# Performance work log

Measured on AMD Instinct MI355X. Metric: run time of the kernel, lower is better.

## Reference

```python
import jax, jax.numpy as jnp
import numpy as np

# dims: bs, closeness, nodes, top-k neighbors, model dim, heads, ffn dim
BS, CLOSE, N, K, D, H, FF = 4, 8, 8192, 16, 64, 4, 256
DH = D // H  # per-head dim


def setup_inputs() -> dict:
    key = jax.random.key(0)
    ks = jax.random.split(key, 7)
    w = lambda k, shp: jax.random.normal(k, shp, jnp.float32) * 0.05
    return {
        "x_c": jax.random.normal(ks[0], (BS, CLOSE, 2, N), jnp.float32),
        "W_emb": w(ks[1], (CLOSE, D)),
        "W_qkv": w(ks[2], (3, D, D)),
        "W_o": w(ks[3], (D, D)),
        "W_ff1": w(ks[4], (D, FF)),
        "W_ff2": w(ks[5], (FF, D)),
        "W_out": w(ks[6], (D, CLOSE)),
    }


def _layernorm(x):
    m = jnp.mean(x, -1, keepdims=True)
    v = jnp.var(x, -1, keepdims=True)
    return (x - m) * jax.lax.rsqrt(v + 1e-5)


def reference(x_c, W_emb, W_qkv, W_o, W_ff1, W_ff2, W_out):
    bs, closeness, _, n = x_c.shape
    # x: bs,2,N,closeness  (x_c.permute(0,2,3,1))
    x = jnp.transpose(x_c, (0, 2, 3, 1)).astype(jnp.float32)
    x0 = x[:, 0]  # bs,N,closeness (feature channel 0)

    # --- getA_cosin: cosine-similarity adjacency, bs x N x N ---
    xn = x0 / (jnp.linalg.norm(x0, axis=-1, keepdims=True) + 1e-12)
    A = jnp.einsum("bmc,bnc->bmn", xn, xn)  # bs,N,N

    # --- index = argsort(A, descending)[:, :, :k]  ->  lax.top_k ---
    _, index = jax.lax.top_k(A, K)  # bs,N,K int32

    # --- vectorized per-node neighbor gather (replaces the bs*N python loop) ---
    # sx[i, j] = x0[i, index[i, j]]  ->  bs,N,K,closeness
    sx = jax.vmap(lambda xb, ib: xb[ib])(x0, index)

    # --- tgt (x_c_2 is None path): x[:,0].unsqueeze(-2) -> bs,N,1,closeness ---
    tgt = x0[:, :, None, :]

    # --- spatial transformer: tgt (len 1) cross-attends over k neighbors ---
    src_e = sx @ W_emb   # bs,N,K,D
    tgt_e = tgt @ W_emb  # bs,N,1,D
    q = tgt_e @ W_qkv[0]
    k_ = src_e @ W_qkv[1]
    v = src_e @ W_qkv[2]
    qh = q.reshape(bs, n, 1, H, DH)
    kh = k_.reshape(bs, n, K, H, DH)
    vh = v.reshape(bs, n, K, H, DH)
    att = jnp.einsum("bnqhd,bnkhd->bnhqk", qh, kh) / jnp.sqrt(jnp.float32(DH))
    p = jax.nn.softmax(att, axis=-1)
    o = jnp.einsum("bnhqk,bnkhd->bnqhd", p, vh).reshape(bs, n, 1, D)
    h1 = _layernorm(tgt_e + o @ W_o)
    h2 = _layernorm(h1 + jax.nn.relu(h1 @ W_ff1) @ W_ff2)
    sq_c = (h2 @ W_out)[:, :, 0, :]  # bs,N,closeness  (squeeze(-2))

    # tgt.permute(0,2,3,1).squeeze(1): (bs,N,1,c) -> (bs,1,c,N) -> (bs,c,N)
    tgt_out = jnp.transpose(tgt, (0, 2, 3, 1))[:, 0]
    return sq_c, tgt_out
```

## Files before the change

kernel.cpp:

```cpp
#include <hip/hip_runtime.h>
#include <hip/hip_fp16.h>

#define BSZ 4
#define CCH 8
#define NN  8192
#define KK  16
#define DD  64
#define HHD 4
#define FFD 256
#define NT  (BSZ*NN)

#define WS_X0   0
#define WS_XN   (WS_X0 + NT*CCH)
#define WS_IDX  (WS_XN + NT*CCH)
#define WS_M    (WS_IDX + NT*KK)
#define WS_EVO  (WS_M + 256)
#define WS_H1   (WS_EVO + 2048)

__global__ __launch_bounds__(256) void k_fusew(const float* __restrict__ Wemb,
                                               const float* __restrict__ Wqkv,
                                               const float* __restrict__ Wo,
                                               float* __restrict__ Mout,
                                               float* __restrict__ Wevo) {
  __shared__ float eq[512], ek[512], ev[512];
  int tid = threadIdx.x;
  for (int i = tid; i < 1536; i += 256) {
    int w = i >> 9;
    int r = i & 511;
    int c = r >> 6, d = r & 63;
    float s = 0.f;
    for (int e = 0; e < 64; ++e) s = fmaf(Wemb[c*64+e], Wqkv[w*4096 + e*64 + d], s);
    float* dst = (w == 0) ? eq : ((w == 1) ? ek : ev);
    dst[r] = s;
  }
  __syncthreads();
  for (int i = tid; i < 256; i += 256) {
    int h = i >> 6, cp = (i >> 3) & 7, c = i & 7;
    float s = 0.f;
    for (int dd = 0; dd < 16; ++dd) s = fmaf(eq[cp*64 + h*16 + dd], ek[c*64 + h*16 + dd], s);
    Mout[i] = s;
  }
  for (int i = tid; i < 2048; i += 256) {
    int hc = i >> 6, dp = i & 63;
    int h = hc >> 3, c = hc & 7;
    float s = 0.f;
    for (int dd = 0; dd < 16; ++dd) s = fmaf(ev[c*64 + h*16 + dd], Wo[(h*16 + dd)*64 + dp], s);
    Wevo[i] = s;
  }
}

__global__ __launch_bounds__(256) void k_prep(const float* __restrict__ xc,
                                              float* __restrict__ x0,
                                              float* __restrict__ xn,
                                              float* __restrict__ outT) {
  int g = blockIdx.x * 256 + threadIdx.x;
  int b = g >> 13, n = g & (NN - 1);
  float v[8];
  float ss = 0.f;
#pragma unroll
  for (int c = 0; c < 8; ++c) {
    float t = xc[((size_t)(b*8 + c) * 2) * NN + n];
    v[c] = t; ss = fmaf(t, t, ss);
  }
  float inv = 1.f / (sqrtf(ss) + 1e-12f);
#pragma unroll
  for (int c = 0; c < 8; ++c) {
    x0[(size_t)g*8 + c] = v[c];
    xn[(size_t)g*8 + c] = v[c] * inv;
    outT[(size_t)b*8*NN + (size_t)c*NN + n] = v[c];
  }
}

#define TPK_R   8
#define TPK_NB  512
#define TPK_CAP 192

__global__ __launch_bounds__(256, 2) void k_topk(const float* __restrict__ xn,
                                                 int* __restrict__ idxo) {
  __shared__ int   hist[TPK_R][TPK_NB];
  __shared__ float scv[TPK_R][TPK_CAP];
  __shared__ int   sci[TPK_R][TPK_CAP];
  __shared__ int   sB[TPK_R];
  __shared__ int   scnt[TPK_R];
  const int tid = threadIdx.x;
  const int rowbase = blockIdx.x * TPK_R;
  const int b = rowbase >> 13;
  const int m0 = rowbase & (NN - 1);
  const float* xnb = xn + (size_t)b * NN * 8;

  float qv[TPK_R][8];
#pragma unroll
  for (int r = 0; r < TPK_R; ++r) {
    const float4* qp = (const float4*)(xnb + (size_t)(m0 + r) * 8);
    float4 a = qp[0], c = qp[1];
    qv[r][0]=a.x; qv[r][1]=a.y; qv[r][2]=a.z; qv[r][3]=a.w;
    qv[r][4]=c.x; qv[r][5]=c.y; qv[r][6]=c.z; qv[r][7]=c.w;
  }
  for (int i = tid; i < TPK_R*TPK_NB; i += 256) ((int*)hist)[i] = 0;
  if (tid < TPK_R) scnt[tid] = 0;
  __syncthreads();

  for (int j = tid; j < NN; j += 256) {
    const float4* xp = (const float4*)(xnb + (size_t)j * 8);
    float4 a = xp[0], c = xp[1];
#pragma unroll
    for (int r = 0; r < TPK_R; ++r) {
      float v = a.x * qv[r][0];
      v = fmaf(a.y, qv[r][1], v); v = fmaf(a.z, qv[r][2], v); v = fmaf(a.w, qv[r][3], v);
      v = fmaf(c.x, qv[r][4], v); v = fmaf(c.y, qv[r][5], v);
      v = fmaf(c.z, qv[r][6], v); v = fmaf(c.w, qv[r][7], v);
      int bb = (int)((v + 1.0f) * 256.0f);
      bb = bb < 0 ? 0 : (bb > (TPK_NB-1) ? (TPK_NB-1) : bb);
      atomicAdd(&hist[r][bb], 1);
    }
  }
  __syncthreads();

  if (tid < TPK_R) {
    int cum = 0, bin = TPK_NB - 1;
    for (;;) {
      cum += hist[tid][bin];
      if (cum >= KK || bin == 0) break;
      --bin;
    }
    sB[tid] = bin;
  }
  __syncthreads();

  for (int j = tid; j < NN; j += 256) {
    const float4* xp = (const float4*)(xnb + (size_t)j * 8);
    float4 a = xp[0], c = xp[1];
#pragma unroll
    for (int r = 0; r < TPK_R; ++r) {
      float v = a.x * qv[r][0];
      v = fmaf(a.y, qv[r][1], v); v = fmaf(a.z, qv[r][2], v); v = fmaf(a.w, qv[r][3], v);
      v = fmaf(c.x, qv[r][4], v); v = fmaf(c.y, qv[r][5], v);
      v = fmaf(c.z, qv[r][6], v); v = fmaf(c.w, qv[r][7], v);
      int bb = (int)((v + 1.0f) * 256.0f);
      bb = bb < 0 ? 0 : (bb > (TPK_NB-1) ? (TPK_NB-1) : bb);
      if (bb >= sB[r]) {
        int p = atomicAdd(&scnt[r], 1);
        if (p < TPK_CAP) { scv[r][p] = v; sci[r][p] = j; }
      }
    }
  }
  __syncthreads();

  {
    int r = tid >> 5, s0 = tid & 31;
    int n = scnt[r]; if (n > TPK_CAP) n = TPK_CAP;
    for (int s = s0; s < n; s += 32) {
      float v = scv[r][s]; int id = sci[r][s];
      int rank = 0;
      for (int t2 = 0; t2 < n; ++t2) {
        float vo = scv[r][t2]; int io = sci[r][t2];
        rank += (vo > v || (vo == v && io < id)) ? 1 : 0;
      }
      if (rank < KK) idxo[(size_t)(rowbase + r)*KK + rank] = id;
    }
  }
}

__global__ __launch_bounds__(256) void k_attn(const float* __restrict__ x0,
                                              const int* __restrict__ idx,
                                              const float* __restrict__ Wemb,
                                              const float* __restrict__ Mw,
                                              const float* __restrict__ Wevo,
                                              float* __restrict__ h1o) {
  __shared__ float sM[256], sE[512], sV[2048];
  int tid = threadIdx.x;
  for (int i = tid; i < 256;  i += 256) sM[i] = Mw[i];
  for (int i = tid; i < 512;  i += 256) sE[i] = Wemb[i];
  for (int i = tid; i < 2048; i += 256) sV[i] = Wevo[i];
  __syncthreads();
  int l = tid & 63;
  int h = l & 3, kk2 = l >> 2;
  int wid = blockIdx.x * 4 + (tid >> 6);
  for (int it = 0; it < 4; ++it) {
    int g = wid * 4 + it;
    int b = g >> 13;
    const float4* xq = (const float4*)(x0 + (size_t)g * 8);
    float4 a0 = xq[0], a1 = xq[1];
    float x0q[8] = {a0.x, a0.y, a0.z, a0.w, a1.x, a1.y, a1.z, a1.w};
    int nk = idx[(size_t)g*KK + kk2];
    const float4* xs = (const float4*)(x0 + ((size_t)(b*NN) + nk) * 8);
    float4 s0 = xs[0], s1v = xs[1];
    float sx[8] = {s0.x, s0.y, s0.z, s0.w, s1v.x, s1v.y, s1v.z, s1v.w};
    float qe[8];
#pragma unroll
    for (int c = 0; c < 8; ++c) {
      float s = 0.f;
#pragma unroll
      for (int c2 = 0; c2 < 8; ++c2) s = fmaf(x0q[c2], sM[h*64 + c2*8 + c], s);
      qe[c] = s;
    }
    float att = 0.f;
#pragma unroll
    for (int c = 0; c < 8; ++c) att = fmaf(sx[c], qe[c], att);
    att *= 0.25f;
    float mx = att;
#pragma unroll
    for (int off = 4; off <= 32; off <<= 1) mx = fmaxf(mx, __shfl_xor(mx, off));
    float e = __expf(att - mx);
    float sum = e;
#pragma unroll
    for (int off = 4; off <= 32; off <<= 1) sum += __shfl_xor(sum, off);
    float p = e / sum;
    float ps[8];
#pragma unroll
    for (int c = 0; c < 8; ++c) ps[c] = p * sx[c];
#pragma unroll
    for (int off = 4; off <= 32; off <<= 1) {
#pragma unroll
      for (int c = 0; c < 8; ++c) ps[c] += __shfl_xor(ps[c], off);
    }
    float r1 = 0.f;
#pragma unroll
    for (int c = 0; c < 8; ++c) {
      float pc = ps[c];
#pragma unroll
      for (int hh = 0; hh < 4; ++hh) {
        float v = __shfl(pc, hh);
        r1 = fmaf(v, sV[(hh*8 + c)*64 + l], r1);
      }
    }
#pragma unroll
    for (int c = 0; c < 8; ++c) r1 = fmaf(x0q[c], sE[c*64 + l], r1);
    float s1 = r1, s2 = r1 * r1;
#pragma unroll
    for (int off = 1; off <= 32; off <<= 1) { s1 += __shfl_xor(s1, off); s2 += __shfl_xor(s2, off); }
    float m = s1 * (1.f/64.f), var = s2 * (1.f/64.f) - m*m;
    float h1v = (r1 - m) * rsqrtf(var + 1e-5f);
    h1o[(size_t)g*DD + l] = h1v;
  }
}

__global__ __launch_bounds__(256) void k_ff(const float* __restrict__ h1,
                                            const float* __restrict__ W1,
                                            const float* __restrict__ W2,
                                            const float* __restrict__ Wout,
                                            float* __restrict__ outp) {
  __shared__ float  h1t[16*64];
  __shared__ __half uh[16*260];
  __shared__ __half w2h[256*66];
  __shared__ float  swout[512];
  __shared__ float  red[16*16*2];
  __shared__ float  red2[16*16*8];
  int tid = threadIdx.x;
  int g0 = blockIdx.x * 16;
  for (int i = tid; i < 1024; i += 256) h1t[i] = h1[(size_t)g0*DD + i];
  {
    int f = tid;
#pragma unroll
    for (int i = 0; i < 64; ++i) w2h[f*66 + i] = __float2half(W2[f*64 + i]);
  }
  for (int i = tid; i < 512; i += 256) swout[i] = Wout[i];
  __syncthreads();
  {
    float w1[64];
#pragma unroll
    for (int d2 = 0; d2 < 64; ++d2) w1[d2] = W1[d2*256 + tid];
    for (int t = 0; t < 16; ++t) {
      float acc = 0.f;
#pragma unroll
      for (int d4 = 0; d4 < 16; ++d4) {
        float4 hv = *(const float4*)&h1t[t*64 + d4*4];
        acc = fmaf(hv.x, w1[d4*4+0], acc);
        acc = fmaf(hv.y, w1[d4*4+1], acc);
        acc = fmaf(hv.z, w1[d4*4+2], acc);
        acc = fmaf(hv.w, w1[d4*4+3], acc);
      }
      uh[t*260 + tid] = __float2half(fmaxf(acc, 0.f));
    }
  }
  __syncthreads();
  int t = tid >> 4, dq = tid & 15, d0 = dq * 4;
  float acc[4];
#pragma unroll
  for (int j = 0; j < 4; ++j) acc[j] = h1t[t*64 + d0 + j];
#pragma unroll 4
  for (int f = 0; f < 256; ++f) {
    float uf = __half2float(uh[t*260 + f]);
#pragma unroll
    for (int j = 0; j < 4; ++j)
      acc[j] = fmaf(uf, __half2float(w2h[f*66 + d0 + j]), acc[j]);
  }
  float s1 = acc[0] + acc[1] + acc[2] + acc[3];
  float s2 = acc[0]*acc[0] + acc[1]*acc[1] + acc[2]*acc[2] + acc[3]*acc[3];
  red[(t*16 + dq)*2 + 0] = s1; red[(t*16 + dq)*2 + 1] = s2;
  __syncthreads();
  float S1 = 0.f, S2 = 0.f;
#pragma unroll
  for (int i = 0; i < 16; ++i) { S1 += red[(t*16 + i)*2]; S2 += red[(t*16 + i)*2 + 1]; }
  float m = S1 * (1.f/64.f), var = S2 * (1.f/64.f) - m*m;
  float rs = rsqrtf(var + 1e-5f);
  float oc[8] = {0,0,0,0,0,0,0,0};
#pragma unroll
  for (int j = 0; j < 4; ++j) {
    float h2 = (acc[j] - m) * rs;
#pragma unroll
    for (int c = 0; c < 8; ++c) oc[c] = fmaf(h2, swout[(d0 + j)*8 + c], oc[c]);
  }
#pragma unroll
  for (int c = 0; c < 8; ++c) red2[(t*16 + dq)*8 + c] = oc[c];
  __syncthreads();
  if (dq < 8) {
    float s = 0.f;
#pragma unroll
    for (int grp = 0; grp < 16; ++grp) s += red2[(t*16 + grp)*8 + dq];
    outp[(size_t)(g0 + t)*8 + dq] = s;
  }
}

extern "C" void kernel_launch(void* const* d_in, const int* in_sizes, int n_in,
                              void* d_out, int out_size, void* d_ws, size_t ws_size,
                              hipStream_t stream) {
  const float* xc   = (const float*)d_in[0];
  const float* Wemb = (const float*)d_in[1];
  const float* Wqkv = (const float*)d_in[2];
  const float* Wo   = (const float*)d_in[3];
  const float* W1   = (const float*)d_in[4];
  const float* W2   = (const float*)d_in[5];
  const float* Wout = (const float*)d_in[6];
  float* out = (float*)d_out;
  float* fw  = (float*)d_ws;
  float* x0  = fw + WS_X0;
  float* xn  = fw + WS_XN;
  int*   idx = (int*)(fw + WS_IDX);
  float* Mw  = fw + WS_M;
  float* Wevo= fw + WS_EVO;
  float* h1  = fw + WS_H1;

  hipLaunchKernelGGL(k_fusew, dim3(1),          dim3(256), 0, stream, Wemb, Wqkv, Wo, Mw, Wevo);
  hipLaunchKernelGGL(k_prep,  dim3(NT/256),     dim3(256), 0, stream, xc, x0, xn, out + (size_t)NT*CCH);
  hipLaunchKernelGGL(k_topk,  dim3(NT/TPK_R),   dim3(256), 0, stream, xn, idx);
  hipLaunchKernelGGL(k_attn,  dim3(2048),       dim3(256), 0, stream, x0, idx, Wemb, Mw, Wevo, h1);
  hipLaunchKernelGGL(k_ff,    dim3(2048),       dim3(256), 0, stream, h1, W1, W2, Wout, out);
}
```

Measured before the change: 315.4 us.

## Use fp16 dot2 scoring for top-k scans with exact fp32 rescoring of candidates

Stores an fp16 copy of the normalized features and runs both top-k scan passes with packed fp16 dot2 instructions. The histogram pass now samples only a quarter of the columns. The threshold search becomes a wave-parallel prefix scan, and it sets a float threshold with a safety margin in place of a bin index. Surviving candidates are rescored in fp32 before ranking, and candidate capacity and occupancy hints are raised. The sampled histogram and fp16 rounding risk overflowing the candidate cap or losing true neighbors, which could silently change the top-k result.

```diff
diff --git a/kernel.cpp b/kernel.cpp
--- a/kernel.cpp
+++ b/kernel.cpp
@@ -16,6 +16,25 @@
 #define WS_M    (WS_IDX + NT*KK)
 #define WS_EVO  (WS_M + 256)
 #define WS_H1   (WS_EVO + 2048)
+#define WS_XNH  (WS_H1 + NT*DD)
+
+typedef _Float16 h2t __attribute__((ext_vector_type(2)));
+
+__device__ __forceinline__ float fdot2_(h2t a, h2t b, float c) {
+#if __has_builtin(__builtin_amdgcn_fdot2)
+  return __builtin_amdgcn_fdot2(a, b, c, false);
+#else
+  return fmaf((float)a[1], (float)b[1], fmaf((float)a[0], (float)b[0], c));
+#endif
+}
+
+__device__ __forceinline__ float dotcol(const uint4 w, const h2t* qh) {
+  float v = fdot2_(__builtin_bit_cast(h2t, w.x), qh[0], 0.f);
+  v = fdot2_(__builtin_bit_cast(h2t, w.y), qh[1], v);
+  v = fdot2_(__builtin_bit_cast(h2t, w.z), qh[2], v);
+  v = fdot2_(__builtin_bit_cast(h2t, w.w), qh[3], v);
+  return v;
+}
 
 __global__ __launch_bounds__(256) void k_fusew(const float* __restrict__ Wemb,
                                                const float* __restrict__ Wqkv,
@@ -52,6 +71,7 @@
 __global__ __launch_bounds__(256) void k_prep(const float* __restrict__ xc,
                                               float* __restrict__ x0,
                                               float* __restrict__ xn,
+                                              _Float16* __restrict__ xnh,
                                               float* __restrict__ outT) {
   int g = blockIdx.x * 256 + threadIdx.x;
   int b = g >> 13, n = g & (NN - 1);
@@ -63,93 +83,128 @@
     v[c] = t; ss = fmaf(t, t, ss);
   }
   float inv = 1.f / (sqrtf(ss) + 1e-12f);
+  float vn[8];
 #pragma unroll
   for (int c = 0; c < 8; ++c) {
+    vn[c] = v[c] * inv;
     x0[(size_t)g*8 + c] = v[c];
-    xn[(size_t)g*8 + c] = v[c] * inv;
+    xn[(size_t)g*8 + c] = vn[c];
     outT[(size_t)b*8*NN + (size_t)c*NN + n] = v[c];
   }
+  uint4 wh;
+  wh.x = __builtin_bit_cast(unsigned, (h2t){(_Float16)vn[0], (_Float16)vn[1]});
+  wh.y = __builtin_bit_cast(unsigned, (h2t){(_Float16)vn[2], (_Float16)vn[3]});
+  wh.z = __builtin_bit_cast(unsigned, (h2t){(_Float16)vn[4], (_Float16)vn[5]});
+  wh.w = __builtin_bit_cast(unsigned, (h2t){(_Float16)vn[6], (_Float16)vn[7]});
+  *(uint4*)(xnh + (size_t)g*8) = wh;
 }
 
 #define TPK_R   8
 #define TPK_NB  512
-#define TPK_CAP 192
-
-__global__ __launch_bounds__(256, 2) void k_topk(const float* __restrict__ xn,
+#define TPK_CAP 320
+
+__global__ __launch_bounds__(256, 4) void k_topk(const float* __restrict__ xn,
+                                                 const _Float16* __restrict__ xnh,
                                                  int* __restrict__ idxo) {
   __shared__ int   hist[TPK_R][TPK_NB];
   __shared__ float scv[TPK_R][TPK_CAP];
   __shared__ int   sci[TPK_R][TPK_CAP];
-  __shared__ int   sB[TPK_R];
+  __shared__ float sQ[TPK_R][8];
+  __shared__ float sT[TPK_R];
   __shared__ int   scnt[TPK_R];
   const int tid = threadIdx.x;
   const int rowbase = blockIdx.x * TPK_R;
   const int b = rowbase >> 13;
   const int m0 = rowbase & (NN - 1);
-  const float* xnb = xn + (size_t)b * NN * 8;
-
-  float qv[TPK_R][8];
+  const float*    xnb = xn  + (size_t)b * NN * 8;
+  const _Float16* xhb = xnh + (size_t)b * NN * 8;
+
+  h2t qh[TPK_R][4];
 #pragma unroll
   for (int r = 0; r < TPK_R; ++r) {
-    const float4* qp = (const float4*)(xnb + (size_t)(m0 + r) * 8);
-    float4 a = qp[0], c = qp[1];
-    qv[r][0]=a.x; qv[r][1]=a.y; qv[r][2]=a.z; qv[r][3]=a.w;
-    qv[r][4]=c.x; qv[r][5]=c.y; qv[r][6]=c.z; qv[r][7]=c.w;
-  }
+    uint4 wq = *(const uint4*)(xhb + (size_t)(m0 + r) * 8);
+    qh[r][0] = __builtin_bit_cast(h2t, wq.x);
+    qh[r][1] = __builtin_bit_cast(h2t, wq.y);
+    qh[r][2] = __builtin_bit_cast(h2t, wq.z);
+    qh[r][3] = __builtin_bit_cast(h2t, wq.w);
+  }
+  if (tid < 64) sQ[tid >> 3][tid & 7] = xnb[(size_t)(m0 + (tid >> 3)) * 8 + (tid & 7)];
   for (int i = tid; i < TPK_R*TPK_NB; i += 256) ((int*)hist)[i] = 0;
   if (tid < TPK_R) scnt[tid] = 0;
   __syncthreads();
 
-  for (int j = tid; j < NN; j += 256) {
-    const float4* xp = (const float4*)(xnb + (size_t)j * 8);
-    float4 a = xp[0], c = xp[1];
+#pragma unroll
+  for (int it = 0; it < 8; ++it) {
+    int j = (it * 256 + tid) * 4;
+    uint4 w = *(const uint4*)(xhb + (size_t)j * 8);
 #pragma unroll
     for (int r = 0; r < TPK_R; ++r) {
-      float v = a.x * qv[r][0];
-      v = fmaf(a.y, qv[r][1], v); v = fmaf(a.z, qv[r][2], v); v = fmaf(a.w, qv[r][3], v);
-      v = fmaf(c.x, qv[r][4], v); v = fmaf(c.y, qv[r][5], v);
-      v = fmaf(c.z, qv[r][6], v); v = fmaf(c.w, qv[r][7], v);
-      int bb = (int)((v + 1.0f) * 256.0f);
+      float v = dotcol(w, qh[r]);
+      int bb = (int)(fmaf(v, 256.f, 256.f));
       bb = bb < 0 ? 0 : (bb > (TPK_NB-1) ? (TPK_NB-1) : bb);
       atomicAdd(&hist[r][bb], 1);
     }
   }
   __syncthreads();
 
-  if (tid < TPK_R) {
-    int cum = 0, bin = TPK_NB - 1;
-    for (;;) {
-      cum += hist[tid][bin];
-      if (cum >= KK || bin == 0) break;
-      --bin;
-    }
-    sB[tid] = bin;
-  }
-  __syncthreads();
-
-  for (int j = tid; j < NN; j += 256) {
-    const float4* xp = (const float4*)(xnb + (size_t)j * 8);
-    float4 a = xp[0], c = xp[1];
+  {
+    int r = tid >> 5, ln = tid & 31;
+    int base = TPK_NB - 1 - ln * 16;
+    int loc = 0;
+#pragma unroll
+    for (int u = 0; u < 16; ++u) loc += hist[r][base - u];
+    int pre = loc;
+#pragma unroll
+    for (int off = 1; off < 32; off <<= 1) {
+      int t2 = __shfl_up(pre, off, 32);
+      if (ln >= off) pre += t2;
+    }
+    int preex = pre - loc;
+    if (preex < KK && pre >= KK) {
+      int cum = preex, bb = base - 15;
+      for (int u = 0; u < 16; ++u) { cum += hist[r][base - u]; if (cum >= KK) { bb = base - u; break; } }
+      sT[r] = fmaf((float)bb, 1.f/256.f, -1.f) - 0.004f;
+    }
+  }
+  __syncthreads();
+  float tr_[TPK_R];
+#pragma unroll
+  for (int r = 0; r < TPK_R; ++r) tr_[r] = sT[r];
+
+  for (int it = 0; it < 32; ++it) {
+    int j = it * 256 + tid;
+    uint4 w = *(const uint4*)(xhb + (size_t)j * 8);
 #pragma unroll
     for (int r = 0; r < TPK_R; ++r) {
-      float v = a.x * qv[r][0];
-      v = fmaf(a.y, qv[r][1], v); v = fmaf(a.z, qv[r][2], v); v = fmaf(a.w, qv[r][3], v);
-      v = fmaf(c.x, qv[r][4], v); v = fmaf(c.y, qv[r][5], v);
-      v = fmaf(c.z, qv[r][6], v); v = fmaf(c.w, qv[r][7], v);
-      int bb = (int)((v + 1.0f) * 256.0f);
-      bb = bb < 0 ? 0 : (bb > (TPK_NB-1) ? (TPK_NB-1) : bb);
-      if (bb >= sB[r]) {
+      float v = dotcol(w, qh[r]);
+      if (v >= tr_[r]) {
         int p = atomicAdd(&scnt[r], 1);
-        if (p < TPK_CAP) { scv[r][p] = v; sci[r][p] = j; }
+        if (p < TPK_CAP) sci[r][p] = j;
       }
     }
   }
   __syncthreads();
 
+#pragma unroll 1
+  for (int r = 0; r < TPK_R; ++r) {
+    int n = scnt[r]; if (n > TPK_CAP) n = TPK_CAP;
+    for (int s = tid; s < n; s += 256) {
+      int j = sci[r][s];
+      const float4* xp = (const float4*)(xnb + (size_t)j * 8);
+      float4 a = xp[0], c = xp[1];
+      float v = a.x * sQ[r][0];
+      v = fmaf(a.y, sQ[r][1], v); v = fmaf(a.z, sQ[r][2], v); v = fmaf(a.w, sQ[r][3], v);
+      v = fmaf(c.x, sQ[r][4], v); v = fmaf(c.y, sQ[r][5], v);
+      v = fmaf(c.z, sQ[r][6], v); v = fmaf(c.w, sQ[r][7], v);
+      scv[r][s] = v;
+    }
+  }
+  __syncthreads();
+
   {
-    int r = tid >> 5, s0 = tid & 31;
+    int r = tid >> 5, l32 = tid & 31;
     int n = scnt[r]; if (n > TPK_CAP) n = TPK_CAP;
-    for (int s = s0; s < n; s += 32) {
+    for (int s = l32; s < n; s += 32) {
       float v = scv[r][s]; int id = sci[r][s];
       int rank = 0;
       for (int t2 = 0; t2 < n; ++t2) {
@@ -330,10 +385,11 @@
   float* Mw  = fw + WS_M;
   float* Wevo= fw + WS_EVO;
   float* h1  = fw + WS_H1;
+  _Float16* xnh = (_Float16*)(fw + WS_XNH);
 
   hipLaunchKernelGGL(k_fusew, dim3(1),          dim3(256), 0, stream, Wemb, Wqkv, Wo, Mw, Wevo);
-  hipLaunchKernelGGL(k_prep,  dim3(NT/256),     dim3(256), 0, stream, xc, x0, xn, out + (size_t)NT*CCH);
-  hipLaunchKernelGGL(k_topk,  dim3(NT/TPK_R),   dim3(256), 0, stream, xn, idx);
+  hipLaunchKernelGGL(k_prep,  dim3(NT/256),     dim3(256), 0, stream, xc, x0, xn, xnh, out + (size_t)NT*CCH);
+  hipLaunchKernelGGL(k_topk,  dim3(NT/TPK_R),   dim3(256), 0, stream, xn, xnh, idx);
   hipLaunchKernelGGL(k_attn,  dim3(2048),       dim3(256), 0, stream, x0, idx, Wemb, Mw, Wevo, h1);
   hipLaunchKernelGGL(k_ff,    dim3(2048),       dim3(256), 0, stream, h1, W1, W2, Wout, out);
 }
```

Measured after the change: 429.5 us. 1.36x slower.
